# Kernel optimization log

Measured on AMD Instinct MI355X. Metric: run time of the kernel, lower is better.

## Reference

```python
import jax, jax.numpy as jnp
import numpy as np

VOCAB, EMB, HID, OUT = 1000, 256, 512, 1
NUM_IN, NUM_OUT = 7, 4
B, S = 64, 512
D = EMB + NUM_OUT  # conv input dim = 260


def setup_inputs() -> dict:
    key = jax.random.key(0)
    ks = jax.random.split(key, 8)
    ev = jax.random.randint(ks[0], (B, S, 1), 0, VOCAB).astype(jnp.float32)
    num = jax.random.normal(ks[1], (B, S, NUM_IN), jnp.float32)
    X = jnp.concatenate([ev, num], axis=-1)  # [B,S,8]; col 0 = event ids
    def w(k, shape, fan_in):
        return jax.random.normal(k, shape, jnp.float32) / np.sqrt(fan_in).astype(np.float32)
    return {
        "X": X,
        "emb": w(ks[2], (VOCAB, EMB), EMB),
        "Wn": w(ks[3], (NUM_IN, NUM_OUT), NUM_IN), "bn": jnp.zeros((NUM_OUT,), jnp.float32),
        "Wf": w(ks[4], (D, 3 * HID), D), "bf": jnp.zeros((3 * HID,), jnp.float32),
        "Wb": w(ks[5], (D, 3 * HID), D), "bb": jnp.zeros((3 * HID,), jnp.float32),
        "Wo": w(ks[6], (2 * HID, OUT), 2 * HID), "bo": jnp.zeros((OUT,), jnp.float32),
    }


def _fo_pool(Z, F):
    # Z, F: [S, B, H]. Linear recurrence h_t = F_t * h_{t-1} + (1 - F_t) * Z_t.
    def step(h, zf):
        z, f = zf
        h = f * h + (1.0 - f) * z
        return h, h
    h0 = jnp.zeros(Z.shape[1:], Z.dtype)
    _, hs = jax.lax.scan(step, h0, (Z, F))
    return hs  # [S, B, H]


def _forward(X, emb, Wn, bn, Wf, bf, Wb, bb, Wo, bo):
    ev = jax.lax.stop_gradient(X[:, :, 0]).astype(jnp.int32)  # event-type ids
    num = X[:, :, 1:]
    e = emb[ev]                          # [B,S,EMB]
    n = num @ Wn + bn                    # [B,S,NUM_OUT]
    c = jnp.concatenate([e, n], axis=-1)  # [B,S,D]

    def gates(W, b):
        g = jnp.einsum('bsd,dk->sbk', c, W) + b  # kernel-1 conv == GEMM; [S,B,3H]
        Z, F = g[..., :HID], g[..., HID:2 * HID]  # O gate is computed but unused upstream
        return jnp.tanh(Z), jax.nn.sigmoid(F)

    Zf, Ff = gates(Wf, bf)
    Zb, Fb = gates(Wb, bb)
    hf = _fo_pool(Zf, Ff)                       # forward direction
    hb = _fo_pool(Zb[::-1], Fb[::-1])[::-1]     # backward: scan reversed, re-reverse
    # torch takes h_combined[-1]: last forward state, first backward-scan state
    final = jnp.concatenate([hf[-1], hb[-1]], axis=-1)  # [B, 2H]
    return final @ Wo + bo  # dropout p=0 is identity


def reference(X, emb, Wn, bn, Wf, bf, Wb, bb, Wo, bo):
    return _forward(X, emb, Wn, bn, Wf, bf, Wb, bb, Wo, bo)
```

## Files before the change

kernel.cpp:

```cpp
#include <hip/hip_runtime.h>
#include <stdint.h>

#define B_ 64
#define S_ 512
#define EMB_ 256
#define NIN_ 7
#define NOUT_ 4
#define HID_ 512
#define VOCAB_ 1000
#define VP_ 1024
#define NG_ 2048

typedef __bf16 bf16x8 __attribute__((ext_vector_type(8)));
typedef float floatx4 __attribute__((ext_vector_type(4)));
typedef unsigned short u16x8 __attribute__((ext_vector_type(8)));

__device__ __forceinline__ unsigned short f2bf(float f) {
    unsigned u = __float_as_uint(f);
    u += 0x7FFFu + ((u >> 16) & 1u);
    return (unsigned short)(u >> 16);
}
__device__ __forceinline__ float bf2f(unsigned short h) {
    return __uint_as_float(((unsigned)h) << 16);
}
__device__ __forceinline__ float rcp_(float x) { return __builtin_amdgcn_rcpf(x); }
__device__ __forceinline__ float exp2_(float x) {
    float r; asm("v_exp_f32 %0, %1" : "=v"(r) : "v"(x)); return r;
}
#define L2E_ 1.4426950408889634f
__device__ __forceinline__ float sigmoidf_(float x) {
    return rcp_(1.0f + exp2_(x * (-L2E_)));
}
__device__ __forceinline__ float tanhf_(float x) {
    float ax = fabsf(x);
    float e = exp2_(ax * (-2.0f * L2E_));
    float t = (1.0f - e) * rcp_(1.0f + e);
    return copysignf(t, x);
}


__device__ __forceinline__ void arrive_(unsigned* c) {
    __syncthreads();
    if (threadIdx.x == 0)
        __hip_atomic_fetch_add(c, 1u, __ATOMIC_RELEASE, __HIP_MEMORY_SCOPE_AGENT);
}
__device__ __forceinline__ void await_(unsigned* c, unsigned target) {
    if (threadIdx.x == 0) {
        while (__hip_atomic_load(c, __ATOMIC_ACQUIRE, __HIP_MEMORY_SCOPE_AGENT) < target)
            __builtin_amdgcn_s_sleep(16);
    }
    __syncthreads();
}

union ShU {
    float raw[32][132];
    struct { float LX[512]; float LN[64][4]; } s;
    float red[8];
};

__global__ __launch_bounds__(512, 4) void mega(
    const float* __restrict__ X, const float* __restrict__ emb,
    const float* __restrict__ Wn, const float* __restrict__ bn,
    const float* __restrict__ Wf, const float* __restrict__ bfv,
    const float* __restrict__ Wb, const float* __restrict__ bb,
    const float* __restrict__ Wo, const float* __restrict__ bo,
    unsigned short* __restrict__ Aemb, unsigned short* __restrict__ WT,
    unsigned short* __restrict__ G, float* __restrict__ W4,
    float* __restrict__ bvec, float* __restrict__ PQ,
    unsigned* __restrict__ bar, float* __restrict__ out, int phase) {
    __shared__ ShU U;
    const int bid = blockIdx.x;
    const int tid = threadIdx.x;
    const bool multi = (phase == 0);

    if (multi || phase == 1) {
        if (bid < 64) {
            int g = bid;
            int t = tid;
            int r15 = t & 15;
            int kchunk = (t >> 4) & 3;
            int kt = t >> 6;
            int row = g * 16 + r15;
            int k0 = kt * 32 + kchunk * 8;
            unsigned short p[8];
            if (row < VOCAB_) {
                float4 a = *(const float4*)(emb + (size_t)row * EMB_ + k0);
                float4 b = *(const float4*)(emb + (size_t)row * EMB_ + k0 + 4);
                p[0]=f2bf(a.x); p[1]=f2bf(a.y); p[2]=f2bf(a.z); p[3]=f2bf(a.w);
                p[4]=f2bf(b.x); p[5]=f2bf(b.y); p[6]=f2bf(b.z); p[7]=f2bf(b.w);
            } else {
#pragma unroll
                for (int q = 0; q < 8; ++q) p[q] = 0;
            }
            size_t chunk = ((size_t)(g >> 3) * 8 + kt) * 8 + (g & 7);
            *(u16x8*)(Aemb + chunk * 512 + (16 * kchunk + r15) * 8) =
                *(const u16x8*)p;
        } else if (bid < 80) {
            int idx = bid - 64;
            int p = idx >> 3;
            int gq = idx & 7;
            const float* W = p ? Wb : Wf;
            int j0 = gq * 64;
            int r = tid >> 3;
            int i = tid & 7;

#pragma unroll
            for (int kt = 0; kt < 8; ++kt) {
                int k0 = kt * 32;
                if (tid < 256) {
                    const float* src = W + (size_t)(k0 + r) * 1536;
                    float4 a0 = *(const float4*)(src + j0 + i * 8);
                    float4 a1 = *(const float4*)(src + j0 + i * 8 + 4);
                    float4 b0 = *(const float4*)(src + 512 + j0 + i * 8);
                    float4 b1 = *(const float4*)(src + 512 + j0 + i * 8 + 4);
                    *(float4*)&U.raw[r][i * 8]          = a0;
                    *(float4*)&U.raw[r][i * 8 + 4]      = a1;
                    *(float4*)&U.raw[r][64 + i * 8]     = b0;
                    *(float4*)&U.raw[r][64 + i * 8 + 4] = b1;
                }
                __syncthreads();
                {
                    int e = tid;
                    int gl = e >> 6;
                    int rest = e & 63;
                    int kchunk = rest >> 4;
                    int v15 = rest & 15;
                    int joff = gl * 8 + (v15 >> 1);
                    int cl = joff + 64 * (v15 & 1);
                    unsigned short pk[8];
#pragma unroll
                    for (int q = 0; q < 8; ++q) pk[q] = f2bf(U.raw[kchunk * 8 + q][cl]);
                    int g = p * 64 + gq * 8 + gl;
                    size_t chunk = ((size_t)(g >> 3) * 8 + kt) * 8 + (g & 7);
                    *(u16x8*)(WT + chunk * 512 + (16 * kchunk + v15) * 8) =
                        *(const u16x8*)pk;
                }
                __syncthreads();
            }
        } else if (bid < 84) {
            int v = (bid - 80) * 512 + tid;
            int part = v >> 10;
            int m = v & 1023;
            int j = m >> 1;
            int c = (m & 1) ? (512 + j) : j;
            const float* W = part ? Wb : Wf;
            float bv = part ? bb[c] : bfv[c];
#pragma unroll
            for (int q = 0; q < NOUT_; ++q) {
                float w = W[(size_t)(256 + q) * 1536 + c];
                W4[(size_t)q * NG_ + v] = w;
                bv = fmaf(bn[q], w, bv);
            }
            bvec[v] = bv;
        }
    }
    if (multi && bid < 84) arrive_(bar + 0);

    if ((multi || phase == 2) && bid < 128) {
        if (multi) await_(bar + 0, 84u);
        int mtile = bid & 7;
        int ntile = bid >> 3;
        int r0 = mtile * 128;
        int n0 = ntile * 128;
        int lane = tid & 63, wave = tid >> 6;
        int wm = wave & 1;
        int wn = wave >> 1;
        int rl = lane & 15;

        const unsigned short* pa = Aemb + ((size_t)mtile * 64 + 4 * wm) * 512 + lane * 8;
        const unsigned short* pb = WT + ((size_t)ntile * 64 + 2 * wn) * 512 + lane * 8;

        floatx4 acc[4][2];
#pragma unroll
        for (int mi = 0; mi < 4; ++mi)
#pragma unroll
            for (int ni = 0; ni < 2; ++ni) acc[mi][ni] = (floatx4){0.f, 0.f, 0.f, 0.f};

        bf16x8 afc[4], bfc[2], afn[4], bfn[2];
#pragma unroll
        for (int mi = 0; mi < 4; ++mi) afc[mi] = *(const bf16x8*)(pa + mi * 512);
#pragma unroll
        for (int ni = 0; ni < 2; ++ni) bfc[ni] = *(const bf16x8*)(pb + ni * 512);

#pragma unroll
        for (int kt = 0; kt < 8; ++kt) {
            if (kt < 7) {
#pragma unroll
                for (int mi = 0; mi < 4; ++mi)
                    afn[mi] = *(const bf16x8*)(pa + (size_t)(kt + 1) * 4096 + mi * 512);
#pragma unroll
                for (int ni = 0; ni < 2; ++ni)
                    bfn[ni] = *(const bf16x8*)(pb + (size_t)(kt + 1) * 4096 + ni * 512);
            }
#pragma unroll
            for (int mi = 0; mi < 4; ++mi)
#pragma unroll
                for (int ni = 0; ni < 2; ++ni)
                    acc[mi][ni] = __builtin_amdgcn_mfma_f32_16x16x32_bf16(afc[mi], bfc[ni], acc[mi][ni], 0, 0, 0);
            if (kt < 7) {
#pragma unroll
                for (int mi = 0; mi < 4; ++mi) afc[mi] = afn[mi];
#pragma unroll
                for (int ni = 0; ni < 2; ++ni) bfc[ni] = bfn[ni];
            }
        }

#pragma unroll
        for (int ni = 0; ni < 2; ++ni) {
            int n = n0 + 32 * wn + 16 * ni + rl;
            float bv = bvec[n];
#pragma unroll
            for (int mi = 0; mi < 4; ++mi) {
                int rb = r0 + 64 * wm + 16 * mi + (lane >> 4) * 4;
#pragma unroll
                for (int v = 0; v < 4; ++v)
                    G[(size_t)(rb + v) * NG_ + n] = f2bf(acc[mi][ni][v] + bv);
            }
        }
    }
    if (multi && bid < 128) arrive_(bar + 1);

    if (multi || phase == 3) {
        if (multi) await_(bar + 1, 128u);
        int b = bid >> 3, chunk = bid & 7;
        int s0 = chunk * 64;
        int j = tid;

        U.s.LX[j] = X[((size_t)b * S_ + s0 + (j >> 3)) * 8 + (j & 7)];
        __syncthreads();

        if (j < 256) {
            int t = j >> 2, q = j & 3;
            float s = 0.f;
#pragma unroll
            for (int i = 0; i < NIN_; ++i)
                s = fmaf(U.s.LX[t * 8 + 1 + i], Wn[i * NOUT_ + q], s);
            U.s.LN[t][q] = s;
        }

        float2 w4p[NOUT_];
#pragma unroll
        for (int q = 0; q < NOUT_; ++q)
            w4p[q] = *(const float2*)(W4 + (size_t)q * NG_ + 2 * j);
        __syncthreads();

        float P = 1.f, Q = 0.f;
        int ev0 = (int)U.s.LX[0];
        unsigned gpA = *(const unsigned*)(G + (size_t)ev0 * NG_ + 2 * j);
        int ev1 = (int)U.s.LX[8];
        unsigned gpB = *(const unsigned*)(G + (size_t)ev1 * NG_ + 2 * j);
#pragma unroll 4
        for (int s = 0; s < 64; ++s) {
            unsigned gpc = gpA;
            gpA = gpB;
            if (s < 62) {
                int evn = (int)U.s.LX[(s + 2) * 8];
                gpB = *(const unsigned*)(G + (size_t)evn * NG_ + 2 * j);
            }
            float gz = bf2f((unsigned short)(gpc & 0xffffu));
            float gf = bf2f((unsigned short)(gpc >> 16));
            float4 n4 = *(const float4*)(&U.s.LN[s][0]);
            gz = fmaf(n4.x, w4p[0].x, gz);
            gz = fmaf(n4.y, w4p[1].x, gz);
            gz = fmaf(n4.z, w4p[2].x, gz);
            gz = fmaf(n4.w, w4p[3].x, gz);
            gf = fmaf(n4.x, w4p[0].y, gf);
            gf = fmaf(n4.y, w4p[1].y, gf);
            gf = fmaf(n4.z, w4p[2].y, gf);
            gf = fmaf(n4.w, w4p[3].y, gf);
            float z = tanhf_(gz);
            float f = sigmoidf_(gf);
            Q = fmaf(f, Q - z, z);
            P *= f;
        }
        ((float2*)PQ)[(size_t)bid * 512 + j] = make_float2(P, Q);
    }
    if (multi) arrive_(bar + 2);

    if ((multi || phase == 4) && bid < 64) {
        if (multi) await_(bar + 2, 512u);
        int b = bid;
        int j = tid;

        float h = 0.f;
#pragma unroll
        for (int c = 0; c < 8; ++c) {
            float2 pq = ((const float2*)PQ)[((size_t)b * 8 + c) * 512 + j];
            h = fmaf(pq.x, h, pq.y);
        }

        const float* xr = X + ((size_t)b * S_ + (S_ - 1)) * 8;
        int ev = (int)xr[0];
        float n4[NOUT_];
#pragma unroll
        for (int q = 0; q < NOUT_; ++q) {
            float s = 0.f;
#pragma unroll
            for (int i = 0; i < NIN_; ++i) s = fmaf(xr[1 + i], Wn[i * NOUT_ + q], s);
            n4[q] = s;
        }
        unsigned gpc = *(const unsigned*)(G + (size_t)ev * NG_ + 1024 + 2 * j);
        float gz = bf2f((unsigned short)(gpc & 0xffffu));
        float gf = bf2f((unsigned short)(gpc >> 16));
#pragma unroll
        for (int q = 0; q < NOUT_; ++q) {
            float2 w = *(const float2*)(W4 + (size_t)q * NG_ + 1024 + 2 * j);
            gz = fmaf(n4[q], w.x, gz);
            gf = fmaf(n4[q], w.y, gf);
        }
        float hb = (1.f - sigmoidf_(gf)) * tanhf_(gz);

        float partial = fmaf(h, Wo[j], hb * Wo[512 + j]);
#pragma unroll
        for (int off = 32; off > 0; off >>= 1)
            partial += __shfl_down(partial, off);
        if ((j & 63) == 0) U.red[j >> 6] = partial;
        __syncthreads();
        if (j == 0) {
            float s = bo[0];
#pragma unroll
            for (int w = 0; w < 8; ++w) s += U.red[w];
            out[b] = s;
        }
    }
}

extern "C" void kernel_launch(void* const* d_in, const int* in_sizes, int n_in,
                              void* d_out, int out_size, void* d_ws, size_t ws_size,
                              hipStream_t stream) {
    const float* X   = (const float*)d_in[0];
    const float* emb = (const float*)d_in[1];
    const float* Wn  = (const float*)d_in[2];
    const float* bn  = (const float*)d_in[3];
    const float* Wf  = (const float*)d_in[4];
    const float* bfv = (const float*)d_in[5];
    const float* Wb  = (const float*)d_in[6];
    const float* bb  = (const float*)d_in[7];
    const float* Wo  = (const float*)d_in[8];
    const float* bo  = (const float*)d_in[9];
    float* out = (float*)d_out;

    size_t off_A   = 0;
    size_t off_WT  = off_A  + (size_t)VP_ * EMB_ * 2;
    size_t off_G   = off_WT + (size_t)NG_ * EMB_ * 2;
    size_t off_W4  = off_G  + (size_t)VP_ * NG_ * 2;
    size_t off_bv  = off_W4 + (size_t)NOUT_ * NG_ * 4;
    size_t off_PQ  = off_bv + (size_t)NG_ * 4;
    size_t off_bar = off_PQ + (size_t)B_ * 8 * 512 * 2 * sizeof(float);
    size_t need    = off_bar + 16;
    if (ws_size < need) return;

    unsigned short* Aemb = (unsigned short*)((char*)d_ws + off_A);
    unsigned short* WT   = (unsigned short*)((char*)d_ws + off_WT);
    unsigned short* G    = (unsigned short*)((char*)d_ws + off_G);
    float*          W4   = (float*)((char*)d_ws + off_W4);
    float*          bvec = (float*)((char*)d_ws + off_bv);
    float*          PQ   = (float*)((char*)d_ws + off_PQ);
    unsigned*       bar  = (unsigned*)((char*)d_ws + off_bar);

    static int coop = -1;
    if (coop < 0) {
        int nb = 0;
        hipError_t e = hipOccupancyMaxActiveBlocksPerMultiprocessor(&nb, mega, 512, 0);
        coop = (e == hipSuccess && nb >= 2) ? 1 : 0;
    }

    hipMemsetAsync((char*)d_ws + off_bar, 0, 16, stream);
    if (coop) {
        mega<<<512, 512, 0, stream>>>(X, emb, Wn, bn, Wf, bfv, Wb, bb, Wo, bo,
                                      Aemb, WT, G, W4, bvec, PQ, bar, out, 0);
    } else {
        for (int p = 1; p <= 4; ++p)
            mega<<<512, 512, 0, stream>>>(X, emb, Wn, bn, Wf, bfv, Wb, bb, Wo, bo,
                                          Aemb, WT, G, W4, bvec, PQ, bar, out, p);
    }
}
```

Measured before the change: 110.6 us.

## Replace final grid barrier with per-batch last-block reduction and overlap prologue

Removes the grid-wide barrier before the final combine phase. Each batch's eight chunk blocks now bump a per-batch counter, and the last one to arrive performs the combine and output projection. The X load and numeric projection are moved ahead of the barrier wait so they overlap with the GEMM phase, and the barriers now use relaxed atomics with explicit fences and a shorter sleep. The risk is memory-ordering correctness: the per-batch counter increment is relaxed and has no release fence after the PQ stores, so the last block may read stale values.

```diff
diff --git a/kernel.cpp b/kernel.cpp
--- a/kernel.cpp
+++ b/kernel.cpp
@@ -14,6 +14,7 @@
 typedef __bf16 bf16x8 __attribute__((ext_vector_type(8)));
 typedef float floatx4 __attribute__((ext_vector_type(4)));
 typedef unsigned short u16x8 __attribute__((ext_vector_type(8)));
+typedef unsigned long long ull;
 
 __device__ __forceinline__ unsigned short f2bf(float f) {
     unsigned u = __float_as_uint(f);
@@ -41,13 +42,16 @@
 
 __device__ __forceinline__ void arrive_(unsigned* c) {
     __syncthreads();
-    if (threadIdx.x == 0)
-        __hip_atomic_fetch_add(c, 1u, __ATOMIC_RELEASE, __HIP_MEMORY_SCOPE_AGENT);
+    if (threadIdx.x == 0) {
+        __builtin_amdgcn_fence(__ATOMIC_RELEASE, "agent");
+        __hip_atomic_fetch_add(c, 1u, __ATOMIC_RELAXED, __HIP_MEMORY_SCOPE_AGENT);
+    }
 }
 __device__ __forceinline__ void await_(unsigned* c, unsigned target) {
     if (threadIdx.x == 0) {
-        while (__hip_atomic_load(c, __ATOMIC_ACQUIRE, __HIP_MEMORY_SCOPE_AGENT) < target)
-            __builtin_amdgcn_s_sleep(16);
+        while (__hip_atomic_load(c, __ATOMIC_RELAXED, __HIP_MEMORY_SCOPE_AGENT) < target)
+            __builtin_amdgcn_s_sleep(8);
+        __builtin_amdgcn_fence(__ATOMIC_ACQUIRE, "agent");
     }
     __syncthreads();
 }
@@ -69,9 +73,11 @@
     float* __restrict__ bvec, float* __restrict__ PQ,
     unsigned* __restrict__ bar, float* __restrict__ out, int phase) {
     __shared__ ShU U;
+    __shared__ unsigned lastf;
     const int bid = blockIdx.x;
     const int tid = threadIdx.x;
     const bool multi = (phase == 0);
+    unsigned* bcnt = bar + 2;
 
     if (multi || phase == 1) {
         if (bid < 64) {
@@ -221,14 +227,12 @@
     if (multi && bid < 128) arrive_(bar + 1);
 
     if (multi || phase == 3) {
-        if (multi) await_(bar + 1, 128u);
         int b = bid >> 3, chunk = bid & 7;
         int s0 = chunk * 64;
         int j = tid;
 
         U.s.LX[j] = X[((size_t)b * S_ + s0 + (j >> 3)) * 8 + (j & 7)];
         __syncthreads();
-
         if (j < 256) {
             int t = j >> 2, q = j & 3;
             float s = 0.f;
@@ -237,12 +241,14 @@
                 s = fmaf(U.s.LX[t * 8 + 1 + i], Wn[i * NOUT_ + q], s);
             U.s.LN[t][q] = s;
         }
+        __syncthreads();
+
+        if (multi) await_(bar + 1, 128u);
 
         float2 w4p[NOUT_];
 #pragma unroll
         for (int q = 0; q < NOUT_; ++q)
             w4p[q] = *(const float2*)(W4 + (size_t)q * NG_ + 2 * j);
-        __syncthreads();
 
         float P = 1.f, Q = 0.f;
         int ev0 = (int)U.s.LX[0];
@@ -273,54 +279,64 @@
             Q = fmaf(f, Q - z, z);
             P *= f;
         }
-        ((float2*)PQ)[(size_t)bid * 512 + j] = make_float2(P, Q);
-    }
-    if (multi) arrive_(bar + 2);
-
-    if ((multi || phase == 4) && bid < 64) {
-        if (multi) await_(bar + 2, 512u);
-        int b = bid;
-        int j = tid;
-
-        float h = 0.f;
-#pragma unroll
-        for (int c = 0; c < 8; ++c) {
-            float2 pq = ((const float2*)PQ)[((size_t)b * 8 + c) * 512 + j];
-            h = fmaf(pq.x, h, pq.y);
-        }
-
-        const float* xr = X + ((size_t)b * S_ + (S_ - 1)) * 8;
-        int ev = (int)xr[0];
-        float n4[NOUT_];
-#pragma unroll
-        for (int q = 0; q < NOUT_; ++q) {
-            float s = 0.f;
-#pragma unroll
-            for (int i = 0; i < NIN_; ++i) s = fmaf(xr[1 + i], Wn[i * NOUT_ + q], s);
-            n4[q] = s;
-        }
-        unsigned gpc = *(const unsigned*)(G + (size_t)ev * NG_ + 1024 + 2 * j);
-        float gz = bf2f((unsigned short)(gpc & 0xffffu));
-        float gf = bf2f((unsigned short)(gpc >> 16));
-#pragma unroll
-        for (int q = 0; q < NOUT_; ++q) {
-            float2 w = *(const float2*)(W4 + (size_t)q * NG_ + 1024 + 2 * j);
-            gz = fmaf(n4[q], w.x, gz);
-            gf = fmaf(n4[q], w.y, gf);
-        }
-        float hb = (1.f - sigmoidf_(gf)) * tanhf_(gz);
-
-        float partial = fmaf(h, Wo[j], hb * Wo[512 + j]);
-#pragma unroll
-        for (int off = 32; off > 0; off >>= 1)
-            partial += __shfl_down(partial, off);
-        if ((j & 63) == 0) U.red[j >> 6] = partial;
+        {
+            union { float2 f; ull q; } pv;
+            pv.f = make_float2(P, Q);
+            __hip_atomic_store((ull*)PQ + (size_t)bid * 512 + j, pv.q,
+                               __ATOMIC_RELAXED, __HIP_MEMORY_SCOPE_AGENT);
+        }
+
         __syncthreads();
-        if (j == 0) {
-            float s = bo[0];
-#pragma unroll
-            for (int w = 0; w < 8; ++w) s += U.red[w];
-            out[b] = s;
+        if (tid == 0) {
+            unsigned old = __hip_atomic_fetch_add(bcnt + b, 1u, __ATOMIC_RELAXED,
+                                                  __HIP_MEMORY_SCOPE_AGENT);
+            lastf = (old == 7u);
+        }
+        __syncthreads();
+
+        if (lastf) {
+            float h = 0.f;
+#pragma unroll
+            for (int c = 0; c < 8; ++c) {
+                union { float2 f; ull q; } pv;
+                pv.q = __hip_atomic_load((const ull*)PQ + ((size_t)b * 8 + c) * 512 + j,
+                                         __ATOMIC_RELAXED, __HIP_MEMORY_SCOPE_AGENT);
+                h = fmaf(pv.f.x, h, pv.f.y);
+            }
+
+            const float* xr = X + ((size_t)b * S_ + (S_ - 1)) * 8;
+            int ev = (int)xr[0];
+            float n4[NOUT_];
+#pragma unroll
+            for (int q = 0; q < NOUT_; ++q) {
+                float s = 0.f;
+#pragma unroll
+                for (int i = 0; i < NIN_; ++i) s = fmaf(xr[1 + i], Wn[i * NOUT_ + q], s);
+                n4[q] = s;
+            }
+            unsigned gpc = *(const unsigned*)(G + (size_t)ev * NG_ + 1024 + 2 * j);
+            float gz = bf2f((unsigned short)(gpc & 0xffffu));
+            float gf = bf2f((unsigned short)(gpc >> 16));
+#pragma unroll
+            for (int q = 0; q < NOUT_; ++q) {
+                float2 w = *(const float2*)(W4 + (size_t)q * NG_ + 1024 + 2 * j);
+                gz = fmaf(n4[q], w.x, gz);
+                gf = fmaf(n4[q], w.y, gf);
+            }
+            float hb = (1.f - sigmoidf_(gf)) * tanhf_(gz);
+
+            float partial = fmaf(h, Wo[j], hb * Wo[512 + j]);
+#pragma unroll
+            for (int off = 32; off > 0; off >>= 1)
+                partial += __shfl_down(partial, off);
+            if ((j & 63) == 0) U.red[j >> 6] = partial;
+            __syncthreads();
+            if (j == 0) {
+                float s = bo[0];
+#pragma unroll
+                for (int w = 0; w < 8; ++w) s += U.red[w];
+                out[b] = s;
+            }
         }
     }
 }
@@ -347,7 +363,7 @@
     size_t off_bv  = off_W4 + (size_t)NOUT_ * NG_ * 4;
     size_t off_PQ  = off_bv + (size_t)NG_ * 4;
     size_t off_bar = off_PQ + (size_t)B_ * 8 * 512 * 2 * sizeof(float);
-    size_t need    = off_bar + 16;
+    size_t need    = off_bar + (2 + 64) * sizeof(unsigned);
     if (ws_size < need) return;
 
     unsigned short* Aemb = (unsigned short*)((char*)d_ws + off_A);
@@ -365,12 +381,12 @@
         coop = (e == hipSuccess && nb >= 2) ? 1 : 0;
     }
 
-    hipMemsetAsync((char*)d_ws + off_bar, 0, 16, stream);
+    hipMemsetAsync((char*)d_ws + off_bar, 0, (2 + 64) * sizeof(unsigned), stream);
     if (coop) {
         mega<<<512, 512, 0, stream>>>(X, emb, Wn, bn, Wf, bfv, Wb, bb, Wo, bo,
                                       Aemb, WT, G, W4, bvec, PQ, bar, out, 0);
     } else {
-        for (int p = 1; p <= 4; ++p)
+        for (int p = 1; p <= 3; ++p)
             mega<<<512, 512, 0, stream>>>(X, emb, Wn, bn, Wf, bfv, Wb, bb, Wo, bo,
                                           Aemb, WT, G, W4, bvec, PQ, bar, out, p);
     }
```

Result: slower. 115.8 us (+4.7%).
